# Kernel optimization log

Hardware: AMD Instinct MI355X
Metric: run time of the kernel (lower is better)

Reference implementation:

```python
import jax, jax.numpy as jnp
import numpy as np

N_HASHES = 8
BUCKET_SIZE = 64


def setup_inputs() -> dict:
    key = jax.random.key(0)
    k1, k2, k3, k4 = jax.random.split(key, 4)
    B, T, D = 32, 4096, 64
    n_buckets = T // BUCKET_SIZE          # 64
    n_colors = 2 * n_buckets              # 128
    q = jax.random.normal(k1, (B, T, D), dtype=jnp.float32)
    k = jax.random.normal(k2, (B, T, D), dtype=jnp.float32)
    v = jax.random.normal(k3, (B, T, D), dtype=jnp.float32)
    proj = jax.random.normal(k4, (D, N_HASHES, n_colors // 2), dtype=jnp.float32)
    return {"q": q, "k": k, "v": v, "proj": proj}


def _hash_vectors(x, proj):
    # x: (b,t,d), proj: (d,r,n_colors//2) -> colors: (b,r,t)
    px = jnp.einsum('btd,drn->brtn', x, proj)
    px = jnp.concatenate([px, -px], axis=-1)
    return jnp.argmax(px, axis=-1)


def _gather_btd(values, indices):
    # values: (b,t,d), indices: (b,r,t) -> (b,r,t,d)
    return jnp.take_along_axis(values[:, None, :, :], indices[..., None], axis=2)


def reference(q, k, v, proj):
    b, t, d = q.shape
    bucket_size = BUCKET_SIZE
    n_buckets = t // bucket_size

    # hashing / sorting done without gradient (torch.no_grad in original)
    qs = jax.lax.stop_gradient(q)
    ks = jax.lax.stop_gradient(k)
    buckets_q = _hash_vectors(qs, proj)          # (b,r,t)
    buckets_k = _hash_vectors(ks, proj)          # (b,r,t)
    sticker_q = jnp.argsort(buckets_q, axis=-1)  # (b,r,t)
    undo_sort_q = jnp.argsort(sticker_q, axis=-1)
    sticker_k = jnp.argsort(buckets_k, axis=-1)

    sq = _gather_btd(q, sticker_q)               # (b,r,t,d)
    sk = _gather_btd(k, sticker_k)
    sv = _gather_btd(v, sticker_k)

    split_bin = lambda x: x.reshape(b, N_HASHES, n_buckets, bucket_size, d)
    bq, bk, bv = map(split_bin, (sq, sk, sv))
    # look one back: each bucket attends to itself and previous bucket
    look_one_back = lambda x: jnp.concatenate([jnp.roll(x, 1, axis=2), x], axis=3)
    bk = look_one_back(bk)                       # (b,r,n,2*bucket,d)
    bv = look_one_back(bv)

    dots = jnp.einsum('brnid,brnjd->brnij', bq, bk) * (d ** -0.5)
    dots_lse = jax.scipy.special.logsumexp(dots, axis=-1, keepdims=True)
    attn = jnp.exp(dots - dots_lse)
    bo = jnp.einsum('brnij,brnjd->brnid', attn, bv)

    so = bo.reshape(b, N_HASHES, t, d)
    slogits = dots_lse.reshape(b, N_HASHES, t)
    # undo the sort
    o = jnp.take_along_axis(so, undo_sort_q[..., None], axis=2)     # (b,r,t,d)
    logits = jnp.take_along_axis(slogits, undo_sort_q, axis=2)[..., None]  # (b,r,t,1)

    # combine hash rounds weighted by their logsumexp
    probs = jnp.exp(logits - jax.scipy.special.logsumexp(logits, axis=1, keepdims=True))
    out = jnp.sum(o * probs, axis=1)             # (b,t,d)
    return out
```

## Files before the change

kernel.cpp:

```cpp
#include <hip/hip_runtime.h>
#include <math.h>

#define BATCH 32
#define TLEN  4096
#define DIM   64
#define NHASH 8
#define NBUCK 64
#define BSIZE 64

typedef __attribute__((ext_vector_type(8))) short short8;
typedef __attribute__((ext_vector_type(8))) unsigned short ushort8;
typedef __attribute__((ext_vector_type(4))) float float4v;
typedef __attribute__((ext_vector_type(4))) unsigned int uint4v;

__device__ inline unsigned short bf16_rne(float x) {
  unsigned u = __float_as_uint(x);
  u += 0x7FFFu + ((u >> 16) & 1u);
  return (unsigned short)(u >> 16);
}
__device__ inline float bf16_to_f32(unsigned short h) {
  return __uint_as_float(((unsigned)h) << 16);
}

__global__ __launch_bounds__(256)
void prep_kernel(const float* __restrict__ proj, unsigned short* __restrict__ pjh,
                 unsigned short* __restrict__ pjl, float* __restrict__ proj_t) {
  const int r = blockIdx.x;
  const int tid = threadIdx.x;
  for (int kk = 0; kk < 16; ++kk) {
    int idx = kk * 256 + tid;
    int d = idx >> 6, nn = idx & 63;
    float val = proj[d * 512 + r * 64 + nn];
    unsigned short hb = bf16_rne(val);
    unsigned short lb = bf16_rne(val - bf16_to_f32(hb));
    int g = d >> 3, e = d & 7;
    int o = (nn << 6) + ((g ^ (nn & 7)) << 3) + e;
    pjh[r * 4096 + o] = hb;
    pjl[r * 4096 + o] = lb;
    proj_t[r * 4096 + nn * 64 + d] = val;
  }
}

__global__ __launch_bounds__(256)
void convert_kernel(const float* __restrict__ q, const float* __restrict__ k,
                    const float* __restrict__ v,
                    unsigned short* __restrict__ qh, unsigned short* __restrict__ ql,
                    unsigned short* __restrict__ kh, unsigned short* __restrict__ kl,
                    unsigned short* __restrict__ vh, int b_off) {
  const size_t idx = (size_t)blockIdx.x * 256 + threadIdx.x;
  const int which = blockIdx.y;
  const size_t soff = ((size_t)b_off * TLEN * DIM) + idx * 8;
  const size_t doff = idx * 8;
  if (which == 0) {
    float4 a = *(const float4*)(q + soff);
    float4 b = *(const float4*)(q + soff + 4);
    float vv[8] = {a.x, a.y, a.z, a.w, b.x, b.y, b.z, b.w};
    ushort8 h8, l8;
#pragma unroll
    for (int j = 0; j < 8; ++j) {
      float s = vv[j] * 0.125f;
      unsigned short hb = bf16_rne(s);
      h8[j] = hb;
      l8[j] = bf16_rne(s - bf16_to_f32(hb));
    }
    *(ushort8*)(qh + doff) = h8;
    *(ushort8*)(ql + doff) = l8;
  } else if (which == 1) {
    float4 a = *(const float4*)(k + soff);
    float4 b = *(const float4*)(k + soff + 4);
    float vv[8] = {a.x, a.y, a.z, a.w, b.x, b.y, b.z, b.w};
    ushort8 h8, l8;
#pragma unroll
    for (int j = 0; j < 8; ++j) {
      unsigned short hb = bf16_rne(vv[j]);
      h8[j] = hb;
      l8[j] = bf16_rne(vv[j] - bf16_to_f32(hb));
    }
    *(ushort8*)(kh + doff) = h8;
    *(ushort8*)(kl + doff) = l8;
  } else {
    float4 a = *(const float4*)(v + soff);
    float4 b = *(const float4*)(v + soff + 4);
    float vv[8] = {a.x, a.y, a.z, a.w, b.x, b.y, b.z, b.w};
    ushort8 h8;
#pragma unroll
    for (int j = 0; j < 8; ++j) h8[j] = bf16_rne(vv[j]);
    *(ushort8*)(vh + doff) = h8;
  }
}

__global__ __launch_bounds__(256, 2)
void hash_kernel(const float* __restrict__ x, const float* __restrict__ proj_t,
                 const unsigned short* __restrict__ pjh,
                 const unsigned short* __restrict__ pjl,
                 int* __restrict__ buckets) {
  __shared__ __align__(16) unsigned short pbh[64 * 64];
  __shared__ __align__(16) unsigned short pbl[64 * 64];

  const int tid = threadIdx.x;
  const int w = tid >> 6;
  const int l = tid & 63;
  const int l15 = l & 15;
  const int qd = l >> 4;
  const int r = blockIdx.y, b = blockIdx.z;
  const int t0 = blockIdx.x << 6;

  const unsigned short* gh = pjh + (size_t)r * 4096;
  const unsigned short* gl = pjl + (size_t)r * 4096;
#pragma unroll
  for (int it = 0; it < 2; ++it) {
    int idx = it * 256 + tid;
    *(short8*)&pbh[idx * 8] = *(const short8*)&gh[idx * 8];
    *(short8*)&pbl[idx * 8] = *(const short8*)&gl[idx * 8];
  }

  const int trow_a = t0 + w * 16 + l15;
  const float* xra = x + ((size_t)b * TLEN + trow_a) * DIM;
  short8 Ahi[2], Alo[2];
  float sxp = 0.f;
#pragma unroll
  for (int ks = 0; ks < 2; ++ks) {
    float4 x0 = *(const float4*)(xra + ks * 32 + qd * 8);
    float4 x1 = *(const float4*)(xra + ks * 32 + qd * 8 + 4);
    sxp += fabsf(x0.x) + fabsf(x0.y) + fabsf(x0.z) + fabsf(x0.w)
         + fabsf(x1.x) + fabsf(x1.y) + fabsf(x1.z) + fabsf(x1.w);
    float v[8] = {x0.x, x0.y, x0.z, x0.w, x1.x, x1.y, x1.z, x1.w};
#pragma unroll
    for (int j = 0; j < 8; ++j) {
      unsigned short hb = bf16_rne(v[j]);
      Ahi[ks][j] = (short)hb;
      Alo[ks][j] = (short)bf16_rne(v[j] - bf16_to_f32(hb));
    }
  }
  sxp += __shfl_xor(sxp, 16, 64);
  sxp += __shfl_xor(sxp, 32, 64);
  __syncthreads();

  float4v Sacc[4];
#pragma unroll
  for (int nt = 0; nt < 4; ++nt) {
    float4v z = {0.f, 0.f, 0.f, 0.f};
    Sacc[nt] = z;
#pragma unroll
    for (int ks = 0; ks < 2; ++ks) {
      int nn = nt * 16 + l15;
      int gk = ks * 4 + qd;
      int o = (nn << 6) + ((gk ^ (nn & 7)) << 3);
      short8 Bh = *(const short8*)&pbh[o];
      short8 Bl = *(const short8*)&pbl[o];
      Sacc[nt] = __builtin_amdgcn_mfma_f32_16x16x32_bf16(Bh, Ahi[ks], Sacc[nt], 0, 0, 0);
      Sacc[nt] = __builtin_amdgcn_mfma_f32_16x16x32_bf16(Bh, Alo[ks], Sacc[nt], 0, 0, 0);
      Sacc[nt] = __builtin_amdgcn_mfma_f32_16x16x32_bf16(Bl, Ahi[ks], Sacc[nt], 0, 0, 0);
      Sacc[nt] = __builtin_amdgcn_mfma_f32_16x16x32_bf16(Bl, Alo[ks], Sacc[nt], 0, 0, 0);
    }
  }

  float bv = -INFINITY, sbv = -INFINITY;
  int bidx = 0;
#pragma unroll
  for (int nt = 0; nt < 4; ++nt) {
#pragma unroll
    for (int i = 0; i < 4; ++i) {
      float d = Sacc[nt][i];
      float a = fabsf(d);
      int idx2 = nt * 16 + qd * 4 + i + (int)((__float_as_uint(d) >> 25) & 64u);
      float nsb = fmaxf(fminf(a, bv), sbv);
      bidx = (a > bv) ? idx2 : bidx;
      bv = fmaxf(a, bv);
      sbv = nsb;
    }
  }
#pragma unroll
  for (int h = 16; h <= 32; h <<= 1) {
    float obv = __shfl_xor(bv, h, 64);
    float osb = __shfl_xor(sbv, h, 64);
    int   obi = __shfl_xor(bidx, h, 64);
    float nsb = fmaxf(fmaxf(sbv, osb), fminf(bv, obv));
    bidx = (obv > bv) ? obi : bidx;
    bv = fmaxf(bv, obv);
    sbv = nsb;
  }

  bool needf = (bv - sbv) < 2.5e-4f * sxp;
  unsigned long long need = __ballot(needf);
  unsigned rows = (unsigned)(need & 0xFFFFull);
  if (rows) {
    const float* pt = proj_t + (size_t)r * 4096;
    while (rows) {
      int rr = __ffs(rows) - 1;
      rows &= rows - 1;
      const float* xr2 = x + ((size_t)b * TLEN + (t0 + w * 16 + rr)) * DIM;
      double s = 0.0;
      for (int d = 0; d < 64; ++d)
        s = fma((double)xr2[d], (double)pt[l * 64 + d], s);
      double b1 = fabs(s);
      int i1 = (s >= -s) ? l : l + 64;
#pragma unroll
      for (int h = 1; h <= 32; h <<= 1) {
        double ob = __shfl_xor(b1, h, 64);
        int    oi = __shfl_xor(i1, h, 64);
        if (ob > b1 || (ob == b1 && oi < i1)) { b1 = ob; i1 = oi; }
      }
      if (l15 == rr) bidx = i1;
    }
  }

  if (qd == 0)
    buckets[((size_t)b * NHASH + r) * TLEN + t0 + w * 16 + l15] = bidx;
}

__global__ __launch_bounds__(64)
void sort_kernel(const int* __restrict__ buckets, int* __restrict__ sticker,
                 int* __restrict__ pos) {
  __shared__ int lhist[64][129];
  __shared__ int starts[128];
  const int lane = threadIdx.x;
  const int br = blockIdx.x;
  const int* bk = buckets + (size_t)br * TLEN;
  int* st = sticker + (size_t)br * TLEN;
  int* ps = pos ? pos + (size_t)br * TLEN : nullptr;

  for (int i = 0; i < 128; ++i) lhist[lane][i] = 0;
  __syncthreads();
  for (int i = 0; i < 64; ++i) lhist[lane][bk[lane * 64 + i]]++;
  __syncthreads();

  int tot0 = 0, tot1 = 0;
  for (int c = 0; c < 64; ++c) {
    int v0 = lhist[c][lane];      lhist[c][lane]      = tot0; tot0 += v0;
    int v1 = lhist[c][lane + 64]; lhist[c][lane + 64] = tot1; tot1 += v1;
  }
  int s0 = tot0;
  for (int off = 1; off < 64; off <<= 1) {
    int u = __shfl_up(s0, off, 64);
    if (lane >= off) s0 += u;
  }
  int total0 = __shfl(s0, 63, 64);
  int s1 = tot1;
  for (int off = 1; off < 64; off <<= 1) {
    int u = __shfl_up(s1, off, 64);
    if (lane >= off) s1 += u;
  }
  starts[lane] = s0 - tot0;
  starts[lane + 64] = s1 - tot1 + total0;
  __syncthreads();

  for (int i = 0; i < 64; ++i) {
    int e = lane * 64 + i;
    int bb = bk[e];
    int c = lhist[lane][bb];
    lhist[lane][bb] = c + 1;
    int sp = starts[bb] + c;
    st[sp] = e;
    if (ps) ps[e] = sp;
  }
}

__global__ __launch_bounds__(256, 2)
void attn_kernel(const unsigned short* __restrict__ qh, const unsigned short* __restrict__ ql,
                 const unsigned short* __restrict__ kh, const unsigned short* __restrict__ kl,
                 const unsigned short* __restrict__ vh,
                 const int* __restrict__ sticker_q, const int* __restrict__ sticker_k,
                 unsigned short* __restrict__ so_buf, float* __restrict__ slse_buf,
                 int b_off) {
  __shared__ __align__(16) unsigned short Khi[128 * 64];
  __shared__ __align__(16) unsigned short Klo[128 * 64];
  __shared__ __align__(16) unsigned short VtS[64 * 128];

  const int tid = threadIdx.x;
  const int w = tid >> 6;
  const int l = tid & 63;
  const int l15 = l & 15;
  const int qd = l >> 4;
  const int n = blockIdx.x, r = blockIdx.y, bl = blockIdx.z;
  const int b = b_off + bl;
  const size_t brbase = ((size_t)b * NHASH + r) * TLEN;
  const size_t obase  = ((size_t)bl * NHASH + r) * TLEN;
  const int nprev = (n + NBUCK - 1) & (NBUCK - 1);

  for (int it = 0; it < 4; ++it) {
    int idx = it * 256 + tid;
    int row = idx >> 3, gc = idx & 7;
    int srow = (row < 64) ? (nprev * 64 + row) : (n * 64 + (row - 64));
    int ik = sticker_k[brbase + srow];
    size_t src = ((size_t)bl * TLEN + ik) * DIM + gc * 8;
    int fr = (row ^ (row >> 1)) & 7;
    int o = (row << 6) + ((gc ^ fr) << 3);
    *(short8*)&Khi[o] = *(const short8*)(kh + src);
    *(short8*)&Klo[o] = *(const short8*)(kl + src);
  }
  for (int it = 0; it < 4; ++it) {
    int idx = it * 256 + tid;
    int key = idx & 127, dg = idx >> 7;
    int srow = (key < 64) ? (nprev * 64 + key) : (n * 64 + (key - 64));
    int ik = sticker_k[brbase + srow];
    ushort8 vv = *(const ushort8*)(vh + ((size_t)bl * TLEN + ik) * DIM + dg * 8);
    int kg = key >> 3, kr = key & 7;
#pragma unroll
    for (int e = 0; e < 8; ++e) {
      int d = dg * 8 + e;
      VtS[d * 128 + ((kg ^ (d & 15)) << 3) + kr] = vv[e];
    }
  }

  const int torig = sticker_q[brbase + n * 64 + w * 16 + l15];
  short8 Ahi[2], Alo[2];
#pragma unroll
  for (int ks = 0; ks < 2; ++ks) {
    size_t src = ((size_t)bl * TLEN + torig) * DIM + ks * 32 + qd * 8;
    Ahi[ks] = *(const short8*)(qh + src);
    Alo[ks] = *(const short8*)(ql + src);
  }
  __syncthreads();

  const int kp = ((l15 >> 2) << 3) + (l15 & 3);
  float4v Sacc[8];
#pragma unroll
  for (int nt = 0; nt < 8; ++nt) {
    float4v z = {0.f, 0.f, 0.f, 0.f};
    Sacc[nt] = z;
    int key = ((nt & 3) << 5) + ((nt >> 2) << 2) + kp;
    int fk = (key ^ (key >> 1)) & 7;
#pragma unroll
    for (int ksd = 0; ksd < 2; ++ksd) {
      int gk = ksd * 4 + qd;
      int o = (key << 6) + ((gk ^ fk) << 3);
      short8 Bh = *(const short8*)&Khi[o];
      short8 Bl = *(const short8*)&Klo[o];
      Sacc[nt] = __builtin_amdgcn_mfma_f32_16x16x32_bf16(Bh, Ahi[ksd], Sacc[nt], 0, 0, 0);
      Sacc[nt] = __builtin_amdgcn_mfma_f32_16x16x32_bf16(Bh, Alo[ksd], Sacc[nt], 0, 0, 0);
      Sacc[nt] = __builtin_amdgcn_mfma_f32_16x16x32_bf16(Bl, Ahi[ksd], Sacc[nt], 0, 0, 0);
    }
  }

  float mA = -INFINITY, mB = -INFINITY;
#pragma unroll
  for (int nt = 0; nt < 8; nt += 2) {
    mA = fmaxf(mA, fmaxf(fmaxf(Sacc[nt][0], Sacc[nt][1]),
                         fmaxf(Sacc[nt][2], Sacc[nt][3])));
    mB = fmaxf(mB, fmaxf(fmaxf(Sacc[nt + 1][0], Sacc[nt + 1][1]),
                         fmaxf(Sacc[nt + 1][2], Sacc[nt + 1][3])));
  }
  float m = fmaxf(mA, mB);
  m = fmaxf(m, __shfl_xor(m, 16, 64));
  m = fmaxf(m, __shfl_xor(m, 32, 64));

  unsigned hw[8][2];
  float Zp0 = 0.f, Zp1 = 0.f, Zp2 = 0.f, Zp3 = 0.f;
#pragma unroll
  for (int nt = 0; nt < 8; ++nt) {
    float e0 = __expf(Sacc[nt][0] - m);
    float e1 = __expf(Sacc[nt][1] - m);
    float e2 = __expf(Sacc[nt][2] - m);
    float e3 = __expf(Sacc[nt][3] - m);
    Zp0 += e0; Zp1 += e1; Zp2 += e2; Zp3 += e3;
    unsigned h0, h1;
    asm("v_cvt_pk_bf16_f32 %0, %1, %2" : "=v"(h0) : "v"(e0), "v"(e1));
    asm("v_cvt_pk_bf16_f32 %0, %1, %2" : "=v"(h1) : "v"(e2), "v"(e3));
    hw[nt][0] = h0; hw[nt][1] = h1;
  }
  float Z = (Zp0 + Zp1) + (Zp2 + Zp3);
  Z += __shfl_xor(Z, 16, 64);
  Z += __shfl_xor(Z, 32, 64);
  const float invZ = 1.0f / Z;
  if (qd == 0)
    slse_buf[brbase + n * 64 + w * 16 + l15] = m + __logf(Z);

  float zr[4];
#pragma unroll
  for (int i = 0; i < 4; ++i) zr[i] = __shfl(invZ, qd * 4 + i, 16);

  short8 PhA[4];
#pragma unroll
  for (int ks = 0; ks < 4; ++ks) {
    union { uint4v u; short8 s; } uh;
    uh.u = (uint4v){hw[ks][0], hw[ks][1], hw[ks + 4][0], hw[ks + 4][1]};
    PhA[ks] = uh.s;
  }

  float4v Oacc[4];
#pragma unroll
  for (int dt = 0; dt < 4; ++dt) { float4v z = {0.f, 0.f, 0.f, 0.f}; Oacc[dt] = z; }
#pragma unroll
  for (int ks = 0; ks < 4; ++ks) {
#pragma unroll
    for (int dt = 0; dt < 4; ++dt) {
      int vrow = dt * 16 + l15;
      int gv = (ks * 4 + qd) ^ (vrow & 15);
      short8 Bv = *(const short8*)&VtS[vrow * 128 + (gv << 3)];
      Oacc[dt] = __builtin_amdgcn_mfma_f32_16x16x32_bf16(PhA[ks], Bv, Oacc[dt], 0, 0, 0);
    }
  }

#pragma unroll
  for (int dt = 0; dt < 4; ++dt) {
#pragma unroll
    for (int i = 0; i < 4; ++i) {
      int orow = n * 64 + w * 16 + qd * 4 + i;
      so_buf[(obase + orow) * DIM + dt * 16 + l15] = bf16_rne(Oacc[dt][i] * zr[i]);
    }
  }
}

__global__ __launch_bounds__(256)
void combine_kernel(const unsigned short* __restrict__ so_buf,
                    const float* __restrict__ slse_buf,
                    const int* __restrict__ pos_q, float* __restrict__ out, int b_off) {
  const size_t tid = (size_t)blockIdx.x * 256 + threadIdx.x;
  const size_t bt = tid >> 3;
  const int g = (int)(tid & 7);
  const size_t bl = bt >> 12;
  const size_t t = bt & 4095;
  const size_t b = b_off + bl;

  int pp[8];
  float l[8];
  float M = -INFINITY;
#pragma unroll
  for (int rr = 0; rr < 8; ++rr) {
    pp[rr] = pos_q[(b * NHASH + rr) * TLEN + t];
    l[rr] = slse_buf[(b * NHASH + rr) * TLEN + pp[rr]];
    M = fmaxf(M, l[rr]);
  }
  float Z = 0.f;
  float w[8];
#pragma unroll
  for (int rr = 0; rr < 8; ++rr) { w[rr] = __expf(l[rr] - M); Z += w[rr]; }
  const float invZ = 1.0f / Z;

  float s[8] = {0.f, 0.f, 0.f, 0.f, 0.f, 0.f, 0.f, 0.f};
#pragma unroll
  for (int rr = 0; rr < 8; ++rr) {
    ushort8 ov = *(const ushort8*)(so_buf +
        ((bl * NHASH + rr) * TLEN + (size_t)pp[rr]) * DIM + g * 8);
#pragma unroll
    for (int j = 0; j < 8; ++j)
      s[j] = fmaf(w[rr], bf16_to_f32(ov[j]), s[j]);
  }
  float* op = out + (b * TLEN + t) * DIM + g * 8;
  float4 o0 = make_float4(s[0] * invZ, s[1] * invZ, s[2] * invZ, s[3] * invZ);
  float4 o1 = make_float4(s[4] * invZ, s[5] * invZ, s[6] * invZ, s[7] * invZ);
  *(float4*)op = o0;
  *(float4*)(op + 4) = o1;
}

extern "C" void kernel_launch(void* const* d_in, const int* in_sizes, int n_in,
                              void* d_out, int out_size, void* d_ws, size_t ws_size,
                              hipStream_t stream) {
  const float* q = (const float*)d_in[0];
  const float* k = (const float*)d_in[1];
  const float* v = (const float*)d_in[2];
  const float* proj = (const float*)d_in[3];
  float* out = (float*)d_out;

  char* ws = (char*)d_ws;
  const size_t MB = (size_t)1 << 20;
  const size_t KB = (size_t)1 << 10;
  int* sticker_q = (int*)(ws + 0 * MB);
  int* sticker_k = (int*)(ws + 4 * MB);
  int* pos_q     = (int*)(ws + 8 * MB);
  float* slse_buf = (float*)(ws + 12 * MB);
  unsigned short* pjh = (unsigned short*)(ws + 16 * MB);
  unsigned short* pjl = (unsigned short*)(ws + 16 * MB + 64 * KB);
  float* proj_t  = (float*)(ws + 16 * MB + 128 * KB);
  int* buckets_q = (int*)(ws + 17 * MB);
  int* buckets_k = (int*)(ws + 21 * MB);

  int CB = 32;
  while (CB > 1 && 17 * MB + (size_t)CB * 13 * MB / 2 > ws_size) CB >>= 1;

  char* chunk = ws + 17 * MB;
  unsigned short* so_buf = (unsigned short*)chunk;
  unsigned short* qh = (unsigned short*)(chunk + (size_t)CB * 4 * MB);
  unsigned short* ql = (unsigned short*)(chunk + (size_t)CB * 9 * MB / 2);
  unsigned short* kh = (unsigned short*)(chunk + (size_t)CB * 5 * MB);
  unsigned short* kl = (unsigned short*)(chunk + (size_t)CB * 11 * MB / 2);
  unsigned short* vh = (unsigned short*)(chunk + (size_t)CB * 6 * MB);

  prep_kernel<<<dim3(NHASH), 256, 0, stream>>>(proj, pjh, pjl, proj_t);
  hash_kernel<<<dim3(TLEN / 64, NHASH, BATCH), 256, 0, stream>>>(q, proj_t, pjh, pjl, buckets_q);
  hash_kernel<<<dim3(TLEN / 64, NHASH, BATCH), 256, 0, stream>>>(k, proj_t, pjh, pjl, buckets_k);
  sort_kernel<<<dim3(BATCH * NHASH), 64, 0, stream>>>(buckets_q, sticker_q, pos_q);
  sort_kernel<<<dim3(BATCH * NHASH), 64, 0, stream>>>(buckets_k, sticker_k, nullptr);

  for (int b_off = 0; b_off < BATCH; b_off += CB) {
    convert_kernel<<<dim3(CB * 128, 3), 256, 0, stream>>>(q, k, v, qh, ql, kh, kl, vh, b_off);
    attn_kernel<<<dim3(NBUCK, NHASH, CB), 256, 0, stream>>>(
        qh, ql, kh, kl, vh, sticker_q, sticker_k, so_buf, slse_buf, b_off);
    combine_kernel<<<dim3(CB * TLEN * 8 / 256), 256, 0, stream>>>(
        so_buf, slse_buf, pos_q, out, b_off);
  }
}
```

Baseline: 478.8 us.

## Loop all hash rounds inside one block and merge q/k hash launches

The hash kernel now processes all 8 hash rounds per block, loading each x tile once and converting it to bf16 hi/lo once, instead of re-reading x per round. Projection tiles for the next round are double-buffered in LDS while the current round computes. The q and k hashing launches are merged into one grid via blockIdx.z. This reduces redundant global reads of x and launch overhead, at the cost of an 8x smaller grid with more serial work per block, plus doubled LDS use and a barrier each round.

```diff
diff --git a/kernel.cpp b/kernel.cpp
--- a/kernel.cpp
+++ b/kernel.cpp
@@ -90,29 +90,23 @@
 }
 
 __global__ __launch_bounds__(256, 2)
-void hash_kernel(const float* __restrict__ x, const float* __restrict__ proj_t,
+void hash_kernel(const float* __restrict__ xq, const float* __restrict__ xk,
+                 const float* __restrict__ proj_t,
                  const unsigned short* __restrict__ pjh,
                  const unsigned short* __restrict__ pjl,
-                 int* __restrict__ buckets) {
-  __shared__ __align__(16) unsigned short pbh[64 * 64];
-  __shared__ __align__(16) unsigned short pbl[64 * 64];
+                 int* __restrict__ buckets_q, int* __restrict__ buckets_k) {
+  __shared__ __align__(16) unsigned short pbh[2][4096];
+  __shared__ __align__(16) unsigned short pbl[2][4096];
 
   const int tid = threadIdx.x;
   const int w = tid >> 6;
   const int l = tid & 63;
   const int l15 = l & 15;
   const int qd = l >> 4;
-  const int r = blockIdx.y, b = blockIdx.z;
+  const int b = blockIdx.y;
+  const float* x = blockIdx.z ? xk : xq;
+  int* buckets = blockIdx.z ? buckets_k : buckets_q;
   const int t0 = blockIdx.x << 6;
-
-  const unsigned short* gh = pjh + (size_t)r * 4096;
-  const unsigned short* gl = pjl + (size_t)r * 4096;
-#pragma unroll
-  for (int it = 0; it < 2; ++it) {
-    int idx = it * 256 + tid;
-    *(short8*)&pbh[idx * 8] = *(const short8*)&gh[idx * 8];
-    *(short8*)&pbl[idx * 8] = *(const short8*)&gl[idx * 8];
-  }
 
   const int trow_a = t0 + w * 16 + l15;
   const float* xra = x + ((size_t)b * TLEN + trow_a) * DIM;
@@ -134,79 +128,102 @@
   }
   sxp += __shfl_xor(sxp, 16, 64);
   sxp += __shfl_xor(sxp, 32, 64);
+
+#pragma unroll
+  for (int it = 0; it < 2; ++it) {
+    int idx = it * 256 + tid;
+    *(short8*)&pbh[0][idx * 8] = *(const short8*)&pjh[idx * 8];
+    *(short8*)&pbl[0][idx * 8] = *(const short8*)&pjl[idx * 8];
+  }
   __syncthreads();
 
-  float4v Sacc[4];
-#pragma unroll
-  for (int nt = 0; nt < 4; ++nt) {
-    float4v z = {0.f, 0.f, 0.f, 0.f};
-    Sacc[nt] = z;
-#pragma unroll
-    for (int ks = 0; ks < 2; ++ks) {
-      int nn = nt * 16 + l15;
-      int gk = ks * 4 + qd;
-      int o = (nn << 6) + ((gk ^ (nn & 7)) << 3);
-      short8 Bh = *(const short8*)&pbh[o];
-      short8 Bl = *(const short8*)&pbl[o];
-      Sacc[nt] = __builtin_amdgcn_mfma_f32_16x16x32_bf16(Bh, Ahi[ks], Sacc[nt], 0, 0, 0);
-      Sacc[nt] = __builtin_amdgcn_mfma_f32_16x16x32_bf16(Bh, Alo[ks], Sacc[nt], 0, 0, 0);
-      Sacc[nt] = __builtin_amdgcn_mfma_f32_16x16x32_bf16(Bl, Ahi[ks], Sacc[nt], 0, 0, 0);
-      Sacc[nt] = __builtin_amdgcn_mfma_f32_16x16x32_bf16(Bl, Alo[ks], Sacc[nt], 0, 0, 0);
-    }
-  }
-
-  float bv = -INFINITY, sbv = -INFINITY;
-  int bidx = 0;
-#pragma unroll
-  for (int nt = 0; nt < 4; ++nt) {
-#pragma unroll
-    for (int i = 0; i < 4; ++i) {
-      float d = Sacc[nt][i];
-      float a = fabsf(d);
-      int idx2 = nt * 16 + qd * 4 + i + (int)((__float_as_uint(d) >> 25) & 64u);
-      float nsb = fmaxf(fminf(a, bv), sbv);
-      bidx = (a > bv) ? idx2 : bidx;
-      bv = fmaxf(a, bv);
+  for (int r = 0; r < NHASH; ++r) {
+    const int cur = r & 1;
+    if (r < NHASH - 1) {
+      const unsigned short* gh = pjh + (size_t)(r + 1) * 4096;
+      const unsigned short* gl = pjl + (size_t)(r + 1) * 4096;
+#pragma unroll
+      for (int it = 0; it < 2; ++it) {
+        int idx = it * 256 + tid;
+        *(short8*)&pbh[cur ^ 1][idx * 8] = *(const short8*)&gh[idx * 8];
+        *(short8*)&pbl[cur ^ 1][idx * 8] = *(const short8*)&gl[idx * 8];
+      }
+    }
+
+    float4v Sacc[4];
+#pragma unroll
+    for (int nt = 0; nt < 4; ++nt) {
+      float4v z = {0.f, 0.f, 0.f, 0.f};
+      Sacc[nt] = z;
+#pragma unroll
+      for (int ks = 0; ks < 2; ++ks) {
+        int nn = nt * 16 + l15;
+        int gk = ks * 4 + qd;
+        int o = (nn << 6) + ((gk ^ (nn & 7)) << 3);
+        short8 Bh = *(const short8*)&pbh[cur][o];
+        short8 Bl = *(const short8*)&pbl[cur][o];
+        Sacc[nt] = __builtin_amdgcn_mfma_f32_16x16x32_bf16(Bh, Ahi[ks], Sacc[nt], 0, 0, 0);
+        Sacc[nt] = __builtin_amdgcn_mfma_f32_16x16x32_bf16(Bh, Alo[ks], Sacc[nt], 0, 0, 0);
+        Sacc[nt] = __builtin_amdgcn_mfma_f32_16x16x32_bf16(Bl, Ahi[ks], Sacc[nt], 0, 0, 0);
+        Sacc[nt] = __builtin_amdgcn_mfma_f32_16x16x32_bf16(Bl, Alo[ks], Sacc[nt], 0, 0, 0);
+      }
+    }
+
+    float bv = -INFINITY, sbv = -INFINITY;
+    int bidx = 0;
+#pragma unroll
+    for (int nt = 0; nt < 4; ++nt) {
+#pragma unroll
+      for (int i = 0; i < 4; ++i) {
+        float d = Sacc[nt][i];
+        float a = fabsf(d);
+        int idx2 = nt * 16 + qd * 4 + i + (int)((__float_as_uint(d) >> 25) & 64u);
+        float nsb = fmaxf(fminf(a, bv), sbv);
+        bidx = (a > bv) ? idx2 : bidx;
+        bv = fmaxf(a, bv);
+        sbv = nsb;
+      }
+    }
+#pragma unroll
+    for (int h = 16; h <= 32; h <<= 1) {
+      float obv = __shfl_xor(bv, h, 64);
+      float osb = __shfl_xor(sbv, h, 64);
+      int   obi = __shfl_xor(bidx, h, 64);
+      float nsb = fmaxf(fmaxf(sbv, osb), fminf(bv, obv));
+      bidx = (obv > bv) ? obi : bidx;
+      bv = fmaxf(bv, obv);
       sbv = nsb;
     }
-  }
-#pragma unroll
-  for (int h = 16; h <= 32; h <<= 1) {
-    float obv = __shfl_xor(bv, h, 64);
-    float osb = __shfl_xor(sbv, h, 64);
-    int   obi = __shfl_xor(bidx, h, 64);
-    float nsb = fmaxf(fmaxf(sbv, osb), fminf(bv, obv));
-    bidx = (obv > bv) ? obi : bidx;
-    bv = fmaxf(bv, obv);
-    sbv = nsb;
-  }
-
-  bool needf = (bv - sbv) < 2.5e-4f * sxp;
-  unsigned long long need = __ballot(needf);
-  unsigned rows = (unsigned)(need & 0xFFFFull);
-  if (rows) {
-    const float* pt = proj_t + (size_t)r * 4096;
-    while (rows) {
-      int rr = __ffs(rows) - 1;
-      rows &= rows - 1;
-      const float* xr2 = x + ((size_t)b * TLEN + (t0 + w * 16 + rr)) * DIM;
-      double s = 0.0;
-      for (int d = 0; d < 64; ++d)
-        s = fma((double)xr2[d], (double)pt[l * 64 + d], s);
-      double b1 = fabs(s);
-      int i1 = (s >= -s) ? l : l + 64;
-#pragma unroll
-      for (int h = 1; h <= 32; h <<= 1) {
-        double ob = __shfl_xor(b1, h, 64);
-        int    oi = __shfl_xor(i1, h, 64);
-        if (ob > b1 || (ob == b1 && oi < i1)) { b1 = ob; i1 = oi; }
+
+    bool needf = (bv - sbv) < 2.5e-4f * sxp;
+    unsigned long long need = __ballot(needf);
+    unsigned rows = (unsigned)(need & 0xFFFFull);
+    if (rows) {
+      const float* pt = proj_t + (size_t)r * 4096;
+      while (rows) {
+        int rr = __ffs(rows) - 1;
+        rows &= rows - 1;
+        const float* xr2 = x + ((size_t)b * TLEN + (t0 + w * 16 + rr)) * DIM;
+        double s = 0.0;
+        for (int d = 0; d < 64; ++d)
+          s = fma((double)xr2[d], (double)pt[l * 64 + d], s);
+        double b1 = fabs(s);
+        int i1 = (s >= -s) ? l : l + 64;
+#pragma unroll
+        for (int h = 1; h <= 32; h <<= 1) {
+          double ob = __shfl_xor(b1, h, 64);
+          int    oi = __shfl_xor(i1, h, 64);
+          if (ob > b1 || (ob == b1 && oi < i1)) { b1 = ob; i1 = oi; }
+        }
+        if (l15 == rr) bidx = i1;
       }
-      if (l15 == rr) bidx = i1;
-    }
-  }
-
-  if (qd == 0)
-    buckets[((size_t)b * NHASH + r) * TLEN + t0 + w * 16 + l15] = bidx;
+    }
+
+    if (qd == 0)
+      buckets[((size_t)b * NHASH + r) * TLEN + t0 + w * 16 + l15] = bidx;
+
+    __syncthreads();
+  }
 }
 
 __global__ __launch_bounds__(64)
@@ -478,8 +495,8 @@
   unsigned short* vh = (unsigned short*)(chunk + (size_t)CB * 6 * MB);
 
   prep_kernel<<<dim3(NHASH), 256, 0, stream>>>(proj, pjh, pjl, proj_t);
-  hash_kernel<<<dim3(TLEN / 64, NHASH, BATCH), 256, 0, stream>>>(q, proj_t, pjh, pjl, buckets_q);
-  hash_kernel<<<dim3(TLEN / 64, NHASH, BATCH), 256, 0, stream>>>(k, proj_t, pjh, pjl, buckets_k);
+  hash_kernel<<<dim3(TLEN / 64, BATCH, 2), 256, 0, stream>>>(
+      q, k, proj_t, pjh, pjl, buckets_q, buckets_k);
   sort_kernel<<<dim3(BATCH * NHASH), 64, 0, stream>>>(buckets_q, sticker_q, pos_q);
   sort_kernel<<<dim3(BATCH * NHASH), 64, 0, stream>>>(buckets_k, sticker_k, nullptr);
 
```

After: 462.2 us. 3.5% less time.
